# Optimization experiments

Hardware: AMD Instinct MI355X
Metric: run time of the kernel (lower is better)

## Reference

```python
import jax, jax.numpy as jnp
import numpy as np

# dims
B, N, DEG = 128, 512, 8          # graphs per batch, nodes per graph, avg degree
NL, F1, F2, F3 = 32, 128, 96, 64  # label dim, GCN filter sizes
K, BINS, BN = 16, 16, 32          # tensor_neurons, bins, bottle_neck_neurons
NT = B * N                        # total nodes per side
E = NT * DEG                      # total edges per side


def setup_inputs() -> dict:
    key = jax.random.key(0)
    ks = jax.random.split(key, 24)
    x1 = jax.random.normal(ks[0], (NT, NL), jnp.float32)
    x2 = jax.random.normal(ks[1], (NT, NL), jnp.float32)
    # edges constrained to stay within each graph's node block
    src1 = jax.random.randint(ks[2], (E,), 0, NT)
    dst1 = (src1 // N) * N + jax.random.randint(ks[3], (E,), 0, N)
    src2 = jax.random.randint(ks[4], (E,), 0, NT)
    dst2 = (src2 // N) * N + jax.random.randint(ks[5], (E,), 0, N)
    edge_index_1 = jnp.stack([src1, dst1]).astype(jnp.int32)
    edge_index_2 = jnp.stack([src2, dst2]).astype(jnp.int32)
    batch = jnp.repeat(jnp.arange(B, dtype=jnp.int32), N)
    s = 0.1
    params = dict(
        Wc1=jax.random.normal(ks[6], (NL, F1), jnp.float32) * s,
        bc1=jnp.zeros((F1,), jnp.float32),
        Wc2=jax.random.normal(ks[7], (F1, F2), jnp.float32) * s,
        bc2=jnp.zeros((F2,), jnp.float32),
        Wc3=jax.random.normal(ks[8], (F2, F3), jnp.float32) * s,
        bc3=jnp.zeros((F3,), jnp.float32),
        Watt=jax.random.normal(ks[9], (F3, F3), jnp.float32) * s,
        Wt=jax.random.normal(ks[10], (F3, F3, K), jnp.float32) * s,
        Wtb=jax.random.normal(ks[11], (K, 2 * F3), jnp.float32) * s,
        tb=jnp.zeros((K,), jnp.float32),
        W1=jax.random.normal(ks[12], (K + BINS, BN), jnp.float32) * s,
        b1=jnp.zeros((BN,), jnp.float32),
        Ws=jax.random.normal(ks[13], (BN, 1), jnp.float32) * s,
        bs=jnp.zeros((1,), jnp.float32),
    )
    return dict(x1=x1, x2=x2, edge_index_1=edge_index_1, edge_index_2=edge_index_2,
                batch_1=batch, batch_2=batch, **params)


def gcn_layer(x, src, dst, W, b):
    # PyG GCNConv: out = D^{-1/2}(A+I)D^{-1/2} (x W) + b
    n = x.shape[0]
    deg = jax.ops.segment_sum(jnp.ones(src.shape[0], x.dtype), dst, num_segments=n) + 1.0
    dinv = jax.lax.rsqrt(deg)
    h = x @ W
    norm = dinv[src] * dinv[dst]
    agg = jax.ops.segment_sum(h[src] * norm[:, None], dst, num_segments=n)
    agg = agg + h * (dinv * dinv)[:, None]  # self-loop term
    return agg + b


def conv_pass(x, src, dst, Wc1, bc1, Wc2, bc2, Wc3, bc3):
    h = jax.nn.relu(gcn_layer(x, src, dst, Wc1, bc1))  # dropout is identity in eval
    h = jax.nn.relu(gcn_layer(h, src, dst, Wc2, bc2))
    return gcn_layer(h, src, dst, Wc3, bc3)


def attention_pool(x, batch, Watt):
    # SimGNN attention: sigmoid(x . tanh(mean_g(x) W)) weighted sum per graph
    cnt = jax.ops.segment_sum(jnp.ones(x.shape[0], x.dtype), batch, num_segments=B)
    mean = jax.ops.segment_sum(x, batch, num_segments=B) / cnt[:, None]
    ctx = jnp.tanh(mean @ Watt)                       # [B, F3]
    coef = jax.nn.sigmoid(jnp.sum(x * ctx[batch], -1))  # [NT]
    return jax.ops.segment_sum(x * coef[:, None], batch, num_segments=B)


def histogram(f1, f2):
    # all graphs have exactly N nodes -> dense batch is a reshape, num_nodes=N
    f1d = f1.reshape(B, N, F3)
    f2d = f2.reshape(B, N, F3)
    s = jax.lax.stop_gradient(jnp.einsum('bnf,bmf->bnm', f1d, f2d))  # detach
    v = jax.nn.sigmoid(s).reshape(B, N * N)
    vmin = v.min(1, keepdims=True)
    vmax = v.max(1, keepdims=True)
    width = (vmax - vmin) / BINS  # torch.histc with min=max=0 uses data range
    safe = jnp.where(width > 0, width, 1.0)
    idx = jnp.clip(jnp.floor((v - vmin) / safe), 0, BINS - 1).astype(jnp.int32)
    flat = (idx + jnp.arange(B, dtype=jnp.int32)[:, None] * BINS).reshape(-1)
    hist = jax.ops.segment_sum(jnp.ones(B * N * N, v.dtype), flat,
                               num_segments=B * BINS).reshape(B, BINS)
    return hist / hist.sum(1, keepdims=True)


def reference(x1, x2, edge_index_1, edge_index_2, batch_1, batch_2,
              Wc1, bc1, Wc2, bc2, Wc3, bc3, Watt, Wt, Wtb, tb, W1, b1, Ws, bs):
    f1 = conv_pass(x1, edge_index_1[0], edge_index_1[1], Wc1, bc1, Wc2, bc2, Wc3, bc3)
    f2 = conv_pass(x2, edge_index_2[0], edge_index_2[1], Wc1, bc1, Wc2, bc2, Wc3, bc3)
    hist = histogram(f1, f2)
    p1 = attention_pool(f1, batch_1, Watt)
    p2 = attention_pool(f2, batch_2, Watt)
    # tensor network: e1^T W[:,:,k] e2 + Wtb [e1;e2] + b
    scoring = jnp.einsum('bi,ijk,bj->bk', p1, Wt, p2)
    block = jnp.concatenate([p1, p2], axis=1) @ Wtb.T
    t = jax.nn.relu(scoring + block + tb)             # [B, K]
    feat = jnp.concatenate([t, hist], axis=1)         # [B, K+BINS]
    h = jax.nn.relu(feat @ W1 + b1)
    return jax.nn.sigmoid(h @ Ws + bs).reshape(-1)    # [B]
```

## Files before the change

### kernel.cpp

```cpp
#include <hip/hip_runtime.h>
#include <math.h>

#define NTOT  65536
#define NEDGE 524288
#define BGR   128
#define NPG   512
#define NL    32
#define F1    128
#define F2    96
#define F3    64
#define KT    16
#define BINS  16
#define BN    32
#define GCAP  6144

typedef unsigned short bf;
typedef __attribute__((ext_vector_type(8))) short sv8;
typedef __attribute__((ext_vector_type(16))) float fv16;

__device__ __forceinline__ float b2f(bf v) { return __uint_as_float(((unsigned)v) << 16); }
__device__ __forceinline__ bf f2b(float f) {
    unsigned u = __float_as_uint(f);
    return (bf)((u + 0x7FFF + ((u >> 16) & 1)) >> 16);
}
__device__ __forceinline__ float sigm(float x) { return 1.f / (1.f + expf(-x)); }
__device__ __forceinline__ void unswizzle(int bid, int nblk, int& g, int& i) {
    int q = bid >> 3;
    g = ((q / nblk) << 3) | (bid & 7);
    i = q % nblk;
}

__global__ __launch_bounds__(256) void init_k(const float* __restrict__ W1, const float* __restrict__ W2,
                                              const float* __restrict__ W3,
                                              bf* __restrict__ T1, bf* __restrict__ T2, bf* __restrict__ T3,
                                              int* __restrict__ gcount) {
    int i = blockIdx.x * 256 + threadIdx.x;
    if (i < 256) gcount[i] = 0;
    if (i < NL * F1) {
        int co = i >> 5, ci = i & 31;
        T1[i] = f2b(W1[ci * F1 + co]);
    } else if (i < NL * F1 + F1 * F2) {
        int i2 = i - NL * F1;
        int co = i2 >> 7, ci = i2 & 127;
        T2[i2] = f2b(W2[ci * F2 + co]);
    } else if (i < NL * F1 + F1 * F2 + F2 * F3) {
        int i3 = i - NL * F1 - F1 * F2;
        int co = i3 / 96, ci = i3 - co * 96;
        T3[i3] = f2b(W3[ci * F3 + co]);
    }
}

__global__ __launch_bounds__(256) void bucket_k(const int* __restrict__ ei1, const int* __restrict__ ei2,
                                                int* __restrict__ gcount, unsigned* __restrict__ bucket) {
    int side = blockIdx.y;
    const int* src = side ? ei2 : ei1;
    const int* dst = src + NEDGE;
    __shared__ int bc[128], bbase[128], bcur[128];
    int t = threadIdx.x;
    if (t < 128) { bc[t] = 0; bcur[t] = 0; }
    __syncthreads();
    int e0 = blockIdx.x * 1024;
    unsigned lp[4];
    int lg[4];
#pragma unroll
    for (int i = 0; i < 4; i++) {
        int e = e0 + i * 256 + t;
        int s = src[e], d = dst[e];
        int g = d >> 9;
        lp[i] = ((unsigned)s << 9) | (unsigned)(d & 511);
        lg[i] = g;
        atomicAdd(&bc[g], 1);
    }
    __syncthreads();
    if (t < 128 && bc[t] > 0) bbase[t] = atomicAdd(&gcount[side * 128 + t], bc[t]);
    __syncthreads();
#pragma unroll
    for (int i = 0; i < 4; i++) {
        int g = lg[i];
        int pos = bbase[g] + atomicAdd(&bcur[g], 1);
        if (pos < GCAP) bucket[((size_t)side * 128 + g) * GCAP + pos] = lp[i];
    }
}

__global__ __launch_bounds__(256) void csr_k(const unsigned* __restrict__ bucket, const int* __restrict__ gcount,
                                             int* __restrict__ off, float* __restrict__ dinv,
                                             unsigned* __restrict__ ecsr) {
    int side = blockIdx.y, g = blockIdx.x, t = threadIdx.x;
    __shared__ int ncnt[512];
    __shared__ int c2[256];
    __shared__ int cur[512];
    __shared__ float dloc[512];
    __shared__ int gs[128];
    ncnt[t] = 0; ncnt[t + 256] = 0;
    if (t < 128) gs[t] = gcount[side * 128 + t];
    __syncthreads();
    for (int o = 1; o < 128; o <<= 1) {
        int v = (t >= o && t < 128) ? gs[t - o] : 0;
        __syncthreads();
        if (t < 128) gs[t] += v;
        __syncthreads();
    }
    int cnt = gcount[side * 128 + g];
    cnt = cnt < GCAP ? cnt : GCAP;
    int base = side * NEDGE + (g > 0 ? gs[g - 1] : 0);
    const unsigned* bk = bucket + ((size_t)side * 128 + g) * GCAP;
    for (int i = t; i < cnt; i += 256) atomicAdd(&ncnt[bk[i] & 511], 1);
    __syncthreads();
    int e0 = ncnt[2 * t], e1 = ncnt[2 * t + 1];
    c2[t] = e0 + e1;
    __syncthreads();
    for (int o = 1; o < 256; o <<= 1) {
        int v = (t >= o) ? c2[t - o] : 0;
        __syncthreads();
        c2[t] += v;
        __syncthreads();
    }
    int ex = c2[t] - (e0 + e1);
    cur[2 * t] = ex;
    cur[2 * t + 1] = ex + e0;
    float d0 = rsqrtf((float)e0 + 1.f), d1 = rsqrtf((float)e1 + 1.f);
    dloc[2 * t] = d0; dloc[2 * t + 1] = d1;
    int node0 = g * NPG + 2 * t;
    int* offs = off + side * (NTOT + 1);
    offs[node0] = base + ex;
    offs[node0 + 1] = base + ex + e0;
    *(float2*)(dinv + (size_t)side * NTOT + node0) = make_float2(d0, d1);
    if (g == BGR - 1 && t == 0) offs[NTOT] = (side + 1) * NEDGE;
    __syncthreads();
    for (int i = t; i < cnt; i += 256) {
        unsigned p = bk[i];
        int dl = p & 511;
        int s = p >> 9;
        int pos = atomicAdd(&cur[dl], 1);
        float nm = dloc[s & 511] * dloc[dl];
        ecsr[base + pos] = (unsigned)s | ((unsigned)f2b(nm) << 16);
    }
}

#define HSTR 136
__global__ __launch_bounds__(256) void aggemm12_k(const float* __restrict__ x1, const float* __restrict__ x2,
                                                  const int* __restrict__ off, const unsigned* __restrict__ ecsr,
                                                  const float* __restrict__ dinv,
                                                  const bf* __restrict__ wt1, const float* __restrict__ bc1,
                                                  const bf* __restrict__ wt2, bf* __restrict__ Yb) {
    __shared__ bf Hs[128 * HSTR];
    int side = blockIdx.y;
    const float* x = side ? x2 : x1;
    const int* offs = off + side * (NTOT + 1);
    const float* dv = dinv + (size_t)side * NTOT;
    bf* Y = Yb + (size_t)side * NTOT * F2;
    int g, ib;
    unswizzle(blockIdx.x, 4, g, ib);
    int wave = threadIdx.x >> 6, lane = threadIdx.x & 63;
    int half = lane >> 5, r = lane & 31;
    int row0 = g * NPG + ib * 128 + wave * 32;
    int n = row0 + r;
    float z[16];
    float d = dv[n];
    float sc = d * d;
    const float* xr = x + (size_t)n * NL + half * 8;
#pragma unroll
    for (int ks = 0; ks < 2; ks++) {
        float4 v0 = *(const float4*)(xr + ks * 16);
        float4 v1 = *(const float4*)(xr + ks * 16 + 4);
        z[ks * 8 + 0] = v0.x * sc; z[ks * 8 + 1] = v0.y * sc;
        z[ks * 8 + 2] = v0.z * sc; z[ks * 8 + 3] = v0.w * sc;
        z[ks * 8 + 4] = v1.x * sc; z[ks * 8 + 5] = v1.y * sc;
        z[ks * 8 + 6] = v1.z * sc; z[ks * 8 + 7] = v1.w * sc;
    }
    int e0 = offs[n], e1 = offs[n + 1];
    for (int j = e0; j < e1; j++) {
        unsigned en = ecsr[j];
        int s = en & 0xFFFF;
        float w = b2f((bf)(en >> 16));
        const float* xs = x + (size_t)s * NL + half * 8;
#pragma unroll
        for (int ks = 0; ks < 2; ks++) {
            float4 u0 = *(const float4*)(xs + ks * 16);
            float4 u1 = *(const float4*)(xs + ks * 16 + 4);
            z[ks * 8 + 0] += w * u0.x; z[ks * 8 + 1] += w * u0.y;
            z[ks * 8 + 2] += w * u0.z; z[ks * 8 + 3] += w * u0.w;
            z[ks * 8 + 4] += w * u1.x; z[ks * 8 + 5] += w * u1.y;
            z[ks * 8 + 6] += w * u1.z; z[ks * 8 + 7] += w * u1.w;
        }
    }
    sv8 a0, a1;
#pragma unroll
    for (int jj = 0; jj < 8; jj++) {
        a0[jj] = (short)f2b(z[jj]);
        a1[jj] = (short)f2b(z[8 + jj]);
    }
#pragma unroll
    for (int nt = 0; nt < F1 / 32; nt++) {
        const bf* Bp = wt1 + (size_t)(nt * 32 + r) * NL + half * 8;
        sv8 b0 = *(const sv8*)(Bp);
        sv8 b1 = *(const sv8*)(Bp + 16);
        fv16 acc;
#pragma unroll
        for (int i = 0; i < 16; i++) acc[i] = 0.f;
        acc = __builtin_amdgcn_mfma_f32_32x32x16_bf16(a0, b0, acc, 0, 0, 0);
        acc = __builtin_amdgcn_mfma_f32_32x32x16_bf16(a1, b1, acc, 0, 0, 0);
        float bv = bc1[nt * 32 + r];
#pragma unroll
        for (int i = 0; i < 16; i++) {
            int rr = (i & 3) + 8 * (i >> 2) + 4 * half;
            Hs[(wave * 32 + rr) * HSTR + nt * 32 + r] = f2b(fmaxf(acc[i] + bv, 0.f));
        }
    }
    sv8 a[8];
#pragma unroll
    for (int k = 0; k < 8; k++)
        a[k] = *(const sv8*)&Hs[(wave * 32 + r) * HSTR + k * 16 + half * 8];
#pragma unroll
    for (int nt = 0; nt < F2 / 32; nt++) {
        const bf* Bp = wt2 + (size_t)(nt * 32 + r) * F1 + half * 8;
        fv16 acc;
#pragma unroll
        for (int i = 0; i < 16; i++) acc[i] = 0.f;
#pragma unroll
        for (int k = 0; k < 8; k++)
            acc = __builtin_amdgcn_mfma_f32_32x32x16_bf16(a[k], *(const sv8*)(Bp + k * 16), acc, 0, 0, 0);
#pragma unroll
        for (int i = 0; i < 16; i++) {
            int rr = (i & 3) + 8 * (i >> 2) + 4 * half;
            Y[(size_t)(row0 + rr) * F2 + nt * 32 + r] = f2b(acc[i]);
        }
    }
}

template <int CIN, int COUT, int BIAS, int RELU>
__global__ __launch_bounds__(256) void gemmm_k(const bf* __restrict__ Xb, const bf* __restrict__ Wt,
                                               const float* __restrict__ bias, bf* __restrict__ outb) {
    int side = blockIdx.y;
    const bf* X = Xb + (size_t)side * NTOT * CIN;
    bf* out = outb + (size_t)side * NTOT * COUT;
    int wave = threadIdx.x >> 6, lane = threadIdx.x & 63;
    int half = lane >> 5, r = lane & 31;
    int row0 = blockIdx.x * 128 + wave * 32;
    const bf* Ap = X + (size_t)(row0 + r) * CIN + half * 8;
    sv8 a[CIN / 16];
#pragma unroll
    for (int k = 0; k < CIN / 16; k++) a[k] = *(const sv8*)(Ap + k * 16);
#pragma unroll
    for (int nt = 0; nt < COUT / 32; nt++) {
        const bf* Bp = Wt + (size_t)(nt * 32 + r) * CIN + half * 8;
        fv16 acc;
#pragma unroll
        for (int i = 0; i < 16; i++) acc[i] = 0.f;
#pragma unroll
        for (int k = 0; k < CIN / 16; k++)
            acc = __builtin_amdgcn_mfma_f32_32x32x16_bf16(a[k], *(const sv8*)(Bp + k * 16), acc, 0, 0, 0);
        float bv = BIAS ? bias[nt * 32 + r] : 0.f;
#pragma unroll
        for (int i = 0; i < 16; i++) {
            int rr = (i & 3) + 8 * (i >> 2) + 4 * half;
            float v = acc[i] + bv;
            if (RELU) v = fmaxf(v, 0.f);
            out[(size_t)(row0 + rr) * COUT + nt * 32 + r] = f2b(v);
        }
    }
}

template <int C, int RELU>
__global__ __launch_bounds__(256) void agg_k(const bf* __restrict__ hinb, const float* __restrict__ bias,
                                             const int* __restrict__ off, const unsigned* __restrict__ ecsr,
                                             const float* __restrict__ dinv, bf* __restrict__ outb) {
    constexpr int C4 = C / 4;
    constexpr int NBLK = NPG * C4 / 256;
    int side = blockIdx.y;
    const bf* hin = hinb + (size_t)side * NTOT * C;
    bf* out = outb + (size_t)side * NTOT * C;
    const int* offs = off + side * (NTOT + 1);
    int g, ib;
    unswizzle(blockIdx.x, NBLK, g, ib);
    int item = ib * 256 + threadIdx.x;
    int node = g * NPG + item / C4;
    int c = (item % C4) * 4;
    float d = dinv[(size_t)side * NTOT + node];
    float sc = d * d;
    ushort4 h = *(const ushort4*)(hin + (size_t)node * C + c);
    float ax = b2f(h.x) * sc, ay = b2f(h.y) * sc, az = b2f(h.z) * sc, aw = b2f(h.w) * sc;
    int e0 = offs[node], e1 = offs[node + 1];
    int j = e0;
    for (; j + 2 <= e1; j += 2) {
        unsigned ena = ecsr[j], enb = ecsr[j + 1];
        int sa = ena & 0xFFFF, sb = enb & 0xFFFF;
        float wa = b2f((bf)(ena >> 16)), wb = b2f((bf)(enb >> 16));
        ushort4 ha = *(const ushort4*)(hin + (size_t)sa * C + c);
        ushort4 hb = *(const ushort4*)(hin + (size_t)sb * C + c);
        ax += wa * b2f(ha.x) + wb * b2f(hb.x);
        ay += wa * b2f(ha.y) + wb * b2f(hb.y);
        az += wa * b2f(ha.z) + wb * b2f(hb.z);
        aw += wa * b2f(ha.w) + wb * b2f(hb.w);
    }
    if (j < e1) {
        unsigned en = ecsr[j];
        int s = en & 0xFFFF;
        float w = b2f((bf)(en >> 16));
        ushort4 hs = *(const ushort4*)(hin + (size_t)s * C + c);
        ax += w * b2f(hs.x); ay += w * b2f(hs.y); az += w * b2f(hs.z); aw += w * b2f(hs.w);
    }
    float4 bv = *(const float4*)(bias + c);
    ax += bv.x; ay += bv.y; az += bv.z; aw += bv.w;
    if (RELU) {
        ax = fmaxf(ax, 0.f); ay = fmaxf(ay, 0.f); az = fmaxf(az, 0.f); aw = fmaxf(aw, 0.f);
    }
    ushort4 o;
    o.x = f2b(ax); o.y = f2b(ay); o.z = f2b(az); o.w = f2b(aw);
    *(ushort4*)(out + (size_t)node * C + c) = o;
}

template <int C>
__global__ __launch_bounds__(256) void aggf_k(const bf* __restrict__ hinb, const float* __restrict__ bias,
                                              const int* __restrict__ off, const unsigned* __restrict__ ecsr,
                                              const float* __restrict__ dinv,
                                              bf* __restrict__ f1, bf* __restrict__ f2) {
    constexpr int C4 = C / 4;
    constexpr int NBLK = NPG * C4 / 256;
    int side = blockIdx.y;
    const bf* hin = hinb + (size_t)side * NTOT * C;
    bf* out = side ? f2 : f1;
    const int* offs = off + side * (NTOT + 1);
    int g, ib;
    unswizzle(blockIdx.x, NBLK, g, ib);
    int item = ib * 256 + threadIdx.x;
    int node = g * NPG + item / C4;
    int c = (item % C4) * 4;
    float d = dinv[(size_t)side * NTOT + node];
    float sc = d * d;
    ushort4 h = *(const ushort4*)(hin + (size_t)node * C + c);
    float ax = b2f(h.x) * sc, ay = b2f(h.y) * sc, az = b2f(h.z) * sc, aw = b2f(h.w) * sc;
    int e0 = offs[node], e1 = offs[node + 1];
    int j = e0;
    for (; j + 2 <= e1; j += 2) {
        unsigned ena = ecsr[j], enb = ecsr[j + 1];
        int sa = ena & 0xFFFF, sb = enb & 0xFFFF;
        float wa = b2f((bf)(ena >> 16)), wb = b2f((bf)(enb >> 16));
        ushort4 ha = *(const ushort4*)(hin + (size_t)sa * C + c);
        ushort4 hb = *(const ushort4*)(hin + (size_t)sb * C + c);
        ax += wa * b2f(ha.x) + wb * b2f(hb.x);
        ay += wa * b2f(ha.y) + wb * b2f(hb.y);
        az += wa * b2f(ha.z) + wb * b2f(hb.z);
        aw += wa * b2f(ha.w) + wb * b2f(hb.w);
    }
    if (j < e1) {
        unsigned en = ecsr[j];
        int s = en & 0xFFFF;
        float w = b2f((bf)(en >> 16));
        ushort4 hs = *(const ushort4*)(hin + (size_t)s * C + c);
        ax += w * b2f(hs.x); ay += w * b2f(hs.y); az += w * b2f(hs.z); aw += w * b2f(hs.w);
    }
    float4 bv = *(const float4*)(bias + c);
    ax += bv.x; ay += bv.y; az += bv.z; aw += bv.w;
    ushort4 o;
    o.x = f2b(ax); o.y = f2b(ay); o.z = f2b(az); o.w = f2b(aw);
    *(ushort4*)(out + (size_t)node * C + c) = o;
}

__device__ __forceinline__ void sim_tile(const bf* __restrict__ f1, const bf* __restrict__ f2,
                                         int g, int mt, int wave, int lane, fv16 acc[4]) {
    int half = lane >> 5, r = lane & 31;
    const bf* Ap = f1 + ((size_t)g * NPG + mt * 32 + r) * F3 + half * 8;
    sv8 a0 = *(const sv8*)(Ap +  0);
    sv8 a1 = *(const sv8*)(Ap + 16);
    sv8 a2 = *(const sv8*)(Ap + 32);
    sv8 a3 = *(const sv8*)(Ap + 48);
#pragma unroll
    for (int j = 0; j < 4; j++) {
        int nt = j * 4 + wave;
        const bf* Bp = f2 + ((size_t)g * NPG + nt * 32 + r) * F3 + half * 8;
#pragma unroll
        for (int i = 0; i < 16; i++) acc[j][i] = 0.f;
        acc[j] = __builtin_amdgcn_mfma_f32_32x32x16_bf16(a0, *(const sv8*)(Bp +  0), acc[j], 0, 0, 0);
        acc[j] = __builtin_amdgcn_mfma_f32_32x32x16_bf16(a1, *(const sv8*)(Bp + 16), acc[j], 0, 0, 0);
        acc[j] = __builtin_amdgcn_mfma_f32_32x32x16_bf16(a2, *(const sv8*)(Bp + 32), acc[j], 0, 0, 0);
        acc[j] = __builtin_amdgcn_mfma_f32_32x32x16_bf16(a3, *(const sv8*)(Bp + 48), acc[j], 0, 0, 0);
    }
}

__global__ __launch_bounds__(256) void simmean_k(const bf* __restrict__ f1, const bf* __restrict__ f2,
                                                 float* __restrict__ statmin, float* __restrict__ statmax,
                                                 float* __restrict__ meanp) {
    __shared__ float red[256];
    int bid = blockIdx.x;
    int t = threadIdx.x, wave = t >> 6, lane = t & 63;
    if (bid < 2048) {
        int g, mt;
        unswizzle(bid, 16, g, mt);
        fv16 acc[4];
        sim_tile(f1, f2, g, mt, wave, lane, acc);
        float mn = 1e30f, mx = -1e30f;
#pragma unroll
        for (int j = 0; j < 4; j++)
#pragma unroll
            for (int i = 0; i < 16; i++) {
                mn = fminf(mn, acc[j][i]);
                mx = fmaxf(mx, acc[j][i]);
            }
        for (int o = 32; o; o >>= 1) {
            mn = fminf(mn, __shfl_down(mn, o));
            mx = fmaxf(mx, __shfl_down(mx, o));
        }
        if (lane == 0) { red[wave] = mn; red[4 + wave] = mx; }
        __syncthreads();
        if (t == 0) {
            statmin[g * 16 + mt] = fminf(fminf(red[0], red[1]), fminf(red[2], red[3]));
            statmax[g * 16 + mt] = fmaxf(fmaxf(red[4], red[5]), fmaxf(red[6], red[7]));
        }
    } else {
        int idx = bid - 2048;
        int side = idx >> 10, rem = idx & 1023;
        int ch = rem >> 7, g = rem & 127;
        const bf* xp = (side ? f2 : f1) + ((size_t)g * NPG + ch * 64) * F3;
        int f = t & 63;
        float m = 0.f;
#pragma unroll 4
        for (int i = 0; i < 16; i++) m += b2f(xp[(size_t)(wave * 16 + i) * F3 + f]);
        red[t] = m;
        __syncthreads();
        if (t < 64) meanp[(((size_t)side * BGR + g) * 8 + ch) * 64 + t] =
            red[t] + red[64 + t] + red[128 + t] + red[192 + t];
    }
}

__global__ __launch_bounds__(256) void simhctx_k(const bf* __restrict__ f1, const bf* __restrict__ f2,
                                                 const float* __restrict__ statmin, const float* __restrict__ statmax,
                                                 int* __restrict__ hist_p,
                                                 const float* __restrict__ meanp, const float* __restrict__ Watt,
                                                 float* __restrict__ ctxb) {
    __shared__ int ph[256 * 17];
    __shared__ int pr[256];
    int bid = blockIdx.x;
    int t = threadIdx.x, wave = t >> 6, lane = t & 63;
    if (bid < 2048) {
        int g, mt;
        unswizzle(bid, 16, g, mt);
#pragma unroll
        for (int b = 0; b < BINS; b++) ph[t * 17 + b] = 0;
        float pm = (lane < 16) ? statmin[g * 16 + lane] : 1e30f;
        float px = (lane < 16) ? statmax[g * 16 + lane] : -1e30f;
        for (int o = 8; o; o >>= 1) {
            pm = fminf(pm, __shfl_down(pm, o));
            px = fmaxf(px, __shfl_down(px, o));
        }
        float vmin = sigm(__shfl(pm, 0));
        float vmax = sigm(__shfl(px, 0));
        float width = (vmax - vmin) / (float)BINS;
        float inv = 1.0f / (width > 0.f ? width : 1.0f);
        fv16 acc[4];
        sim_tile(f1, f2, g, mt, wave, lane, acc);
#pragma unroll
        for (int j = 0; j < 4; j++)
#pragma unroll
            for (int i = 0; i < 16; i++) {
                float v = sigm(acc[j][i]);
                int bi = (int)floorf((v - vmin) * inv);
                bi = bi < 0 ? 0 : (bi > BINS - 1 ? BINS - 1 : bi);
                ph[t * 17 + bi] += 1;
            }
        __syncthreads();
        {
            int grp = t >> 4, bin = t & 15;
            int s = 0;
#pragma unroll
            for (int j = 0; j < 16; j++) s += ph[(grp * 16 + j) * 17 + bin];
            pr[t] = s;
        }
        __syncthreads();
        if (t < BINS) {
            int tot = 0;
#pragma unroll
            for (int j = 0; j < 16; j++) tot += pr[j * 16 + t];
            hist_p[((size_t)g * 16 + mt) * BINS + t] = tot;
        }
    } else {
        int idx = bid - 2048;
        int side = idx >> 7, g = idx & 127;
        float* sm = (float*)pr;
        if (t < 64) {
            float m = 0.f;
#pragma unroll
            for (int ch = 0; ch < 8; ch++) m += meanp[(((size_t)side * BGR + g) * 8 + ch) * 64 + t];
            sm[t] = m * (1.0f / (float)NPG);
        }
        __syncthreads();
        if (t < 64) {
            float acc = 0.f;
#pragma unroll 8
            for (int i = 0; i < F3; i++) acc += sm[i] * Watt[i * F3 + t];
            ctxb[((size_t)side * BGR + g) * F3 + t] = tanhf(acc);
        }
    }
}

__global__ __launch_bounds__(256) void cpool_k(const bf* __restrict__ f1, const bf* __restrict__ f2,
                                               const float* __restrict__ ctxb, float* __restrict__ poolp) {
    int g = blockIdx.x, ch = blockIdx.y, side = blockIdx.z;
    const bf* xp = (side ? f2 : f1) + ((size_t)g * NPG + ch * 64) * F3;
    int t = threadIdx.x, w = t >> 6, f = t & 63;
    float cx = ctxb[((size_t)side * BGR + g) * F3 + f];
    float acc = 0.f;
    for (int i = 0; i < 16; i++) {
        float v = b2f(xp[(size_t)(w * 16 + i) * F3 + f]);
        float d = v * cx;
#pragma unroll
        for (int o = 1; o < 64; o <<= 1) d += __shfl_xor(d, o);
        acc += sigm(d) * v;
    }
    __shared__ float red[256];
    red[t] = acc;
    __syncthreads();
    if (t < 64) poolp[(((size_t)side * BGR + g) * 8 + ch) * 64 + t] =
        red[t] + red[64 + t] + red[128 + t] + red[192 + t];
}

__global__ __launch_bounds__(256) void final_k(const float* __restrict__ poolp,
                                               const float* __restrict__ Wt, const float* __restrict__ Wtb,
                                               const float* __restrict__ tb, const int* __restrict__ hist_p,
                                               const float* __restrict__ W1, const float* __restrict__ b1,
                                               const float* __restrict__ Ws, const float* __restrict__ bs,
                                               float* __restrict__ out) {
    int b = blockIdx.x, t = threadIdx.x;
    __shared__ float cat[128];
    __shared__ float sacc[256];
    __shared__ float feat[32];
    __shared__ float hb[32];
    if (t < 128) {
        int side = t >> 6, f = t & 63;
        float s = 0.f;
#pragma unroll
        for (int ch = 0; ch < 8; ch++) s += poolp[(((size_t)side * BGR + b) * 8 + ch) * 64 + f];
        cat[t] = s;
    }
    __syncthreads();
    int k = t & 15, c = t >> 4;
    float acc = 0.f;
    for (int q = 0; q < 256; q++) {
        int ij = c * 256 + q;
        int i = ij >> 6, j = ij & 63;
        acc += cat[i] * cat[64 + j] * Wt[ij * KT + k];
    }
    sacc[t] = acc;
    __syncthreads();
    if (t < KT) {
        float sc = 0.f;
        for (int c2 = 0; c2 < 16; c2++) sc += sacc[c2 * 16 + t];
        float bt = 0.f;
        for (int i = 0; i < 128; i++) bt += cat[i] * Wtb[t * 128 + i];
        float tv = sc + bt + tb[t];
        feat[t] = tv > 0.f ? tv : 0.f;
        int hsum = 0;
#pragma unroll
        for (int j = 0; j < 16; j++) hsum += hist_p[((size_t)b * 16 + j) * BINS + t];
        feat[KT + t] = (float)hsum * (1.0f / (float)(NPG * NPG));
    }
    __syncthreads();
    if (t < BN) {
        float a = 0.f;
        for (int i = 0; i < KT + BINS; i++) a += feat[i] * W1[i * BN + t];
        a += b1[t];
        hb[t] = a > 0.f ? a : 0.f;
    }
    __syncthreads();
    if (t == 0) {
        float s = bs[0];
        for (int j = 0; j < BN; j++) s += hb[j] * Ws[j];
        out[b] = sigm(s);
    }
}

extern "C" void kernel_launch(void* const* d_in, const int* in_sizes, int n_in,
                              void* d_out, int out_size, void* d_ws, size_t ws_size,
                              hipStream_t stream) {
    const float* x1   = (const float*)d_in[0];
    const float* x2   = (const float*)d_in[1];
    const int*   ei1  = (const int*)d_in[2];
    const int*   ei2  = (const int*)d_in[3];
    const float* Wc1  = (const float*)d_in[6];
    const float* bc1  = (const float*)d_in[7];
    const float* Wc2  = (const float*)d_in[8];
    const float* bc2  = (const float*)d_in[9];
    const float* Wc3  = (const float*)d_in[10];
    const float* bc3  = (const float*)d_in[11];
    const float* Watt = (const float*)d_in[12];
    const float* Wt   = (const float*)d_in[13];
    const float* Wtb  = (const float*)d_in[14];
    const float* tb   = (const float*)d_in[15];
    const float* W1   = (const float*)d_in[16];
    const float* b1   = (const float*)d_in[17];
    const float* Ws   = (const float*)d_in[18];
    const float* bs   = (const float*)d_in[19];
    float* out = (float*)d_out;

    char* wsb = (char*)d_ws;
    size_t o = 0;
    auto alloc = [&](size_t bytes) -> void* {
        void* p = wsb + o;
        o = (o + bytes + 255) & ~(size_t)255;
        return p;
    };
    bf* f1b  = (bf*)alloc((size_t)NTOT * F3 * 2);
    bf* f2b  = (bf*)alloc((size_t)NTOT * F3 * 2);
    bf* X    = (bf*)alloc((size_t)2 * NTOT * F2 * 2);
    bf* Y    = (bf*)alloc((size_t)2 * NTOT * F2 * 2);
    int* off   = (int*)alloc((size_t)2 * (NTOT + 1) * 4);
    unsigned* ecsr = (unsigned*)alloc((size_t)2 * NEDGE * 4);
    unsigned* bucket = (unsigned*)alloc((size_t)2 * 128 * GCAP * 4);
    int* gcount = (int*)alloc(256 * 4);
    float* dinv = (float*)alloc((size_t)2 * NTOT * 4);
    float* statmin = (float*)alloc((size_t)BGR * 16 * 4);
    float* statmax = (float*)alloc((size_t)BGR * 16 * 4);
    int* hist_p = (int*)alloc((size_t)BGR * 16 * BINS * 4);
    float* meanp = (float*)alloc((size_t)2 * BGR * 8 * 64 * 4);
    float* ctx   = (float*)alloc((size_t)2 * BGR * F3 * 4);
    float* poolp = (float*)alloc((size_t)2 * BGR * 8 * 64 * 4);
    bf* wt1 = (bf*)alloc((size_t)NL * F1 * 2);
    bf* wt2 = (bf*)alloc((size_t)F1 * F2 * 2);
    bf* wt3 = (bf*)alloc((size_t)F2 * F3 * 2);
    (void)ws_size; (void)in_sizes; (void)n_in; (void)out_size;

    init_k<<<(NL * F1 + F1 * F2 + F2 * F3 + 255) / 256, 256, 0, stream>>>(Wc1, Wc2, Wc3, wt1, wt2, wt3, gcount);

    bucket_k<<<dim3(NEDGE / 1024, 2), 256, 0, stream>>>(ei1, ei2, gcount, bucket);
    csr_k<<<dim3(BGR, 2), 256, 0, stream>>>(bucket, gcount, off, dinv, ecsr);

    aggemm12_k<<<dim3(NTOT / 128, 2), 256, 0, stream>>>(x1, x2, off, ecsr, dinv, wt1, bc1, wt2, Y);
    agg_k<F2, 1><<<dim3((NTOT * (F2 / 4)) / 256, 2), 256, 0, stream>>>(Y, bc2, off, ecsr, dinv, X);
    gemmm_k<F2, F3, 0, 0><<<dim3(NTOT / 128, 2), 256, 0, stream>>>(X, wt3, nullptr, Y);
    aggf_k<F3><<<dim3((NTOT * (F3 / 4)) / 256, 2), 256, 0, stream>>>(Y, bc3, off, ecsr, dinv, f1b, f2b);

    simmean_k<<<4096, 256, 0, stream>>>(f1b, f2b, statmin, statmax, meanp);
    simhctx_k<<<2048 + 256, 256, 0, stream>>>(f1b, f2b, statmin, statmax, hist_p, meanp, Watt, ctx);
    cpool_k<<<dim3(BGR, 8, 2), 256, 0, stream>>>(f1b, f2b, ctx, poolp);

    final_k<<<BGR, 256, 0, stream>>>(poolp, Wt, Wtb, tb, hist_p, W1, b1, Ws, bs, out);
}
```

Before: 322.5 us.

## Fuse third GCN layer: aggregate inputs first, then GEMM in one kernel

Replaces the separate layer-3 GEMM kernel and aggregation kernel with one kernel. It aggregates the 96-wide input features over the CSR neighbours in registers, converts them to bf16 and feeds them directly into MFMA with the weight matrix, then adds the bias. This uses (A·X)·W in place of A·(X·W). It removes one launch and the round trip of the intermediate Y buffer, but it gathers 96-wide rows instead of 64-wide ones and each lane holds 48 floats of partial sums, which may raise register pressure. Each lane also walks its own node's edges serially, so per-node work is less parallel.

```diff
diff --git a/kernel.cpp b/kernel.cpp
--- a/kernel.cpp
+++ b/kernel.cpp
@@ -224,39 +224,6 @@
         for (int i = 0; i < 16; i++) {
             int rr = (i & 3) + 8 * (i >> 2) + 4 * half;
             Y[(size_t)(row0 + rr) * F2 + nt * 32 + r] = f2b(acc[i]);
-        }
-    }
-}
-
-template <int CIN, int COUT, int BIAS, int RELU>
-__global__ __launch_bounds__(256) void gemmm_k(const bf* __restrict__ Xb, const bf* __restrict__ Wt,
-                                               const float* __restrict__ bias, bf* __restrict__ outb) {
-    int side = blockIdx.y;
-    const bf* X = Xb + (size_t)side * NTOT * CIN;
-    bf* out = outb + (size_t)side * NTOT * COUT;
-    int wave = threadIdx.x >> 6, lane = threadIdx.x & 63;
-    int half = lane >> 5, r = lane & 31;
-    int row0 = blockIdx.x * 128 + wave * 32;
-    const bf* Ap = X + (size_t)(row0 + r) * CIN + half * 8;
-    sv8 a[CIN / 16];
-#pragma unroll
-    for (int k = 0; k < CIN / 16; k++) a[k] = *(const sv8*)(Ap + k * 16);
-#pragma unroll
-    for (int nt = 0; nt < COUT / 32; nt++) {
-        const bf* Bp = Wt + (size_t)(nt * 32 + r) * CIN + half * 8;
-        fv16 acc;
-#pragma unroll
-        for (int i = 0; i < 16; i++) acc[i] = 0.f;
-#pragma unroll
-        for (int k = 0; k < CIN / 16; k++)
-            acc = __builtin_amdgcn_mfma_f32_32x32x16_bf16(a[k], *(const sv8*)(Bp + k * 16), acc, 0, 0, 0);
-        float bv = BIAS ? bias[nt * 32 + r] : 0.f;
-#pragma unroll
-        for (int i = 0; i < 16; i++) {
-            int rr = (i & 3) + 8 * (i >> 2) + 4 * half;
-            float v = acc[i] + bv;
-            if (RELU) v = fmaxf(v, 0.f);
-            out[(size_t)(row0 + rr) * COUT + nt * 32 + r] = f2b(v);
         }
     }
 }
@@ -310,51 +277,65 @@
     *(ushort4*)(out + (size_t)node * C + c) = o;
 }
 
-template <int C>
-__global__ __launch_bounds__(256) void aggf_k(const bf* __restrict__ hinb, const float* __restrict__ bias,
-                                              const int* __restrict__ off, const unsigned* __restrict__ ecsr,
-                                              const float* __restrict__ dinv,
-                                              bf* __restrict__ f1, bf* __restrict__ f2) {
-    constexpr int C4 = C / 4;
-    constexpr int NBLK = NPG * C4 / 256;
+__global__ __launch_bounds__(256) void agggemm3_k(const bf* __restrict__ Xb, const int* __restrict__ off,
+                                                  const unsigned* __restrict__ ecsr, const float* __restrict__ dinv,
+                                                  const bf* __restrict__ wt3, const float* __restrict__ bc3,
+                                                  bf* __restrict__ f1, bf* __restrict__ f2) {
     int side = blockIdx.y;
-    const bf* hin = hinb + (size_t)side * NTOT * C;
+    const bf* X = Xb + (size_t)side * NTOT * F2;
     bf* out = side ? f2 : f1;
     const int* offs = off + side * (NTOT + 1);
+    const float* dv = dinv + (size_t)side * NTOT;
     int g, ib;
-    unswizzle(blockIdx.x, NBLK, g, ib);
-    int item = ib * 256 + threadIdx.x;
-    int node = g * NPG + item / C4;
-    int c = (item % C4) * 4;
-    float d = dinv[(size_t)side * NTOT + node];
+    unswizzle(blockIdx.x, 4, g, ib);
+    int wave = threadIdx.x >> 6, lane = threadIdx.x & 63;
+    int half = lane >> 5, r = lane & 31;
+    int row0 = g * NPG + ib * 128 + wave * 32;
+    int n = row0 + r;
+    float z[48];
+    float d = dv[n];
     float sc = d * d;
-    ushort4 h = *(const ushort4*)(hin + (size_t)node * C + c);
-    float ax = b2f(h.x) * sc, ay = b2f(h.y) * sc, az = b2f(h.z) * sc, aw = b2f(h.w) * sc;
-    int e0 = offs[node], e1 = offs[node + 1];
-    int j = e0;
-    for (; j + 2 <= e1; j += 2) {
-        unsigned ena = ecsr[j], enb = ecsr[j + 1];
-        int sa = ena & 0xFFFF, sb = enb & 0xFFFF;
-        float wa = b2f((bf)(ena >> 16)), wb = b2f((bf)(enb >> 16));
-        ushort4 ha = *(const ushort4*)(hin + (size_t)sa * C + c);
-        ushort4 hb = *(const ushort4*)(hin + (size_t)sb * C + c);
-        ax += wa * b2f(ha.x) + wb * b2f(hb.x);
-        ay += wa * b2f(ha.y) + wb * b2f(hb.y);
-        az += wa * b2f(ha.z) + wb * b2f(hb.z);
-        aw += wa * b2f(ha.w) + wb * b2f(hb.w);
-    }
-    if (j < e1) {
+    const bf* xr = X + (size_t)n * F2 + half * 8;
+#pragma unroll
+    for (int k = 0; k < 6; k++) {
+        sv8 v = *(const sv8*)(xr + k * 16);
+#pragma unroll
+        for (int jj = 0; jj < 8; jj++) z[k * 8 + jj] = b2f((bf)v[jj]) * sc;
+    }
+    int e0 = offs[n], e1 = offs[n + 1];
+    for (int j = e0; j < e1; j++) {
         unsigned en = ecsr[j];
         int s = en & 0xFFFF;
         float w = b2f((bf)(en >> 16));
-        ushort4 hs = *(const ushort4*)(hin + (size_t)s * C + c);
-        ax += w * b2f(hs.x); ay += w * b2f(hs.y); az += w * b2f(hs.z); aw += w * b2f(hs.w);
-    }
-    float4 bv = *(const float4*)(bias + c);
-    ax += bv.x; ay += bv.y; az += bv.z; aw += bv.w;
-    ushort4 o;
-    o.x = f2b(ax); o.y = f2b(ay); o.z = f2b(az); o.w = f2b(aw);
-    *(ushort4*)(out + (size_t)node * C + c) = o;
+        const bf* xs = X + (size_t)s * F2 + half * 8;
+#pragma unroll
+        for (int k = 0; k < 6; k++) {
+            sv8 u = *(const sv8*)(xs + k * 16);
+#pragma unroll
+            for (int jj = 0; jj < 8; jj++) z[k * 8 + jj] += w * b2f((bf)u[jj]);
+        }
+    }
+    sv8 a[6];
+#pragma unroll
+    for (int k = 0; k < 6; k++)
+#pragma unroll
+        for (int jj = 0; jj < 8; jj++) a[k][jj] = (short)f2b(z[k * 8 + jj]);
+#pragma unroll
+    for (int nt = 0; nt < F3 / 32; nt++) {
+        const bf* Bp = wt3 + (size_t)(nt * 32 + r) * F2 + half * 8;
+        fv16 acc;
+#pragma unroll
+        for (int i = 0; i < 16; i++) acc[i] = 0.f;
+#pragma unroll
+        for (int k = 0; k < 6; k++)
+            acc = __builtin_amdgcn_mfma_f32_32x32x16_bf16(a[k], *(const sv8*)(Bp + k * 16), acc, 0, 0, 0);
+        float bv = bc3[nt * 32 + r];
+#pragma unroll
+        for (int i = 0; i < 16; i++) {
+            int rr = (i & 3) + 8 * (i >> 2) + 4 * half;
+            out[(size_t)(row0 + rr) * F3 + nt * 32 + r] = f2b(acc[i] + bv);
+        }
+    }
 }
 
 __device__ __forceinline__ void sim_tile(const bf* __restrict__ f1, const bf* __restrict__ f2,
@@ -626,8 +607,7 @@
 
     aggemm12_k<<<dim3(NTOT / 128, 2), 256, 0, stream>>>(x1, x2, off, ecsr, dinv, wt1, bc1, wt2, Y);
     agg_k<F2, 1><<<dim3((NTOT * (F2 / 4)) / 256, 2), 256, 0, stream>>>(Y, bc2, off, ecsr, dinv, X);
-    gemmm_k<F2, F3, 0, 0><<<dim3(NTOT / 128, 2), 256, 0, stream>>>(X, wt3, nullptr, Y);
-    aggf_k<F3><<<dim3((NTOT * (F3 / 4)) / 256, 2), 256, 0, stream>>>(Y, bc3, off, ecsr, dinv, f1b, f2b);
+    agggemm3_k<<<dim3(NTOT / 128, 2), 256, 0, stream>>>(X, off, ecsr, dinv, wt3, bc3, f1b, f2b);
 
     simmean_k<<<4096, 256, 0, stream>>>(f1b, f2b, statmin, statmax, meanp);
     simhctx_k<<<2048 + 256, 256, 0, stream>>>(f1b, f2b, statmin, statmax, hist_p, meanp, Watt, ctx);
```

After: 327.4 us. Within noise of the previous version (+1.5%).
